# Kernel optimization log

Measured on AMD Instinct MI355X. Metric: run time of the kernel, lower is better.

Reference implementation:

```python
import jax, jax.numpy as jnp
import numpy as np

H = 50      # hidden_size (fixed in source)
IN = 7      # input_size = len(features)
B = 1024    # batch
T = 512     # seq_len
FC1 = 25
OUT = 1


def setup_inputs() -> dict:
    key = jax.random.key(0)
    ks = jax.random.split(key, 24)
    s = 1.0 / np.sqrt(H)  # PyTorch LSTM/Linear default uniform init scale

    def u(k, shape):
        return jax.random.uniform(k, shape, jnp.float32, -s, s)

    d = {"x": jax.random.normal(ks[0], (B, T, IN), jnp.float32)}
    # 4 stacked LSTM layers total: lstm1 has 2 layers (in=7 then 50), lstm2 has 2 layers (in=50)
    in_sizes = [IN, H, H, H]
    for l, isz in enumerate(in_sizes):
        d[f"Wih{l}"] = u(ks[1 + 4 * l], (4 * H, isz))
        d[f"Whh{l}"] = u(ks[2 + 4 * l], (4 * H, H))
        d[f"bih{l}"] = u(ks[3 + 4 * l], (4 * H,))
        d[f"bhh{l}"] = u(ks[4 + 4 * l], (4 * H,))
    d["W1"] = u(ks[17], (FC1, H))
    d["b1"] = u(ks[18], (FC1,))
    d["W2"] = u(ks[19], (OUT, FC1))
    d["b2"] = u(ks[20], (OUT,))
    return d


def _lstm_layer(x, Wih, Whh, bih, bhh):
    # x: [B, T, in] -> hidden sequence [B, T, H]. PyTorch gate order: i, f, g, o.
    b, t, _ = x.shape
    h = Whh.shape[1]
    # Precompute input projection for all timesteps in one big GEMM: [T, B, 4H]
    xp = jnp.einsum('bti,gi->tbg', x, Wih) + (bih + bhh)

    def step(carry, xt):
        hs, cs = carry
        gates = xt + hs @ Whh.T                      # [B, 4H]
        i, f, g, o = jnp.split(gates, 4, axis=-1)
        i = jax.nn.sigmoid(i)
        f = jax.nn.sigmoid(f)
        g = jnp.tanh(g)
        o = jax.nn.sigmoid(o)
        cs = f * cs + i * g
        hs = o * jnp.tanh(cs)
        return (hs, cs), hs

    h0 = jnp.zeros((b, h), x.dtype)
    _, hseq = jax.lax.scan(step, (h0, h0), xp)       # hseq: [T, B, H]
    return hseq.transpose(1, 0, 2)


def reference(x, Wih0, Whh0, bih0, bhh0, Wih1, Whh1, bih1, bhh1,
              Wih2, Whh2, bih2, bhh2, Wih3, Whh3, bih3, bhh3,
              W1, b1, W2, b2):
    out = x
    layers = [(Wih0, Whh0, bih0, bhh0), (Wih1, Whh1, bih1, bhh1),
              (Wih2, Whh2, bih2, bhh2), (Wih3, Whh3, bih3, bhh3)]
    for Wih, Whh, bih, bhh in layers:
        out = _lstm_layer(out, Wih, Whh, bih, bhh)
    h = out[:, -1, :]                                # last timestep [B, H]
    # dropout is identity in eval mode
    h = jax.nn.relu(h @ W1.T + b1)
    return h @ W2.T + b2                             # [B, 1]
```

## Files before the change

### kernel.cpp

```cpp
#include <hip/hip_runtime.h>


#define H 50
#define INSZ 7
#define TT 512
#define NL 4
#define FC1N 25
#define BPG 4
#define NBLK 256
#define NTHREADS 1024
#define HS 80
#define BIASL 56

typedef _Float16 half_t;
typedef __attribute__((ext_vector_type(8))) _Float16 half8_t;
typedef __attribute__((ext_vector_type(4))) float float4_t;

struct Params {
  const float* x;
  const float* Wih[NL];
  const float* Whh[NL];
  const float* bih[NL];
  const float* bhh[NL];
  const float* W1;
  const float* b1;
  const float* W2;
  const float* b2;
  float* out;
};

#define MFMA16(A, B, C) __builtin_amdgcn_mfma_f32_16x16x32_f16((A), (B), (C), 0, 0, 0)
#define EXP2F(x) __builtin_amdgcn_exp2f(x)
#define RCPF(x) __builtin_amdgcn_rcpf(x)

__global__ __launch_bounds__(NTHREADS, 4) void lstm_r10(Params p) {
  __shared__ __align__(16) half_t Xpack[2][BPG][HS];
  __shared__ __align__(16) half_t Hbuf[3][2][BPG][HS];
  __shared__ __align__(16) half_t Xstage[64][BPG][8];
  __shared__ float fc_h[BPG][H];
  __shared__ float fc1_buf[BPG][FC1N];

  const int tid = threadIdx.x;
  const int b0 = blockIdx.x * BPG;
  const int lane = tid & 63;
  const int quad = lane >> 4;
  const int col = lane & 15;
  const int glay = tid >> 8;
  const int wl = (((tid >> 6) & 3) + glay) & 3;

  half8_t afrag[4][4];
#pragma unroll
  for (int t4 = 0; t4 < 4; ++t4) {
#pragma unroll
    for (int g = 0; g < 4; ++g) {
      half8_t v;
#pragma unroll
      for (int j = 0; j < 8; ++j) {
        const int r = wl * 64 + t4 * 16 + col;
        const int u = r >> 2, q = r & 3;
        const int k = g * 32 + quad * 8 + j;
        float wv = 0.0f;
        if (u < H) {
          const int row = q * H + u;
          if (glay == 0) {
            if (k < INSZ) wv = p.Wih[0][row * INSZ + k];
            else if (k == 7) wv = p.bih[0][row] + p.bhh[0][row];
            else if (k >= 8 && k < 8 + H) wv = p.Whh[0][row * H + (k - 8)];
          } else if (glay == 1) {
            if (k == 7) wv = p.bih[1][row] + p.bhh[1][row];
            else if (k >= 8 && k < 8 + H) wv = p.Wih[1][row * H + (k - 8)];
            else if (k >= 64 && k < 64 + H) wv = p.Whh[1][row * H + (k - 64)];
          } else {
            if (k < H) wv = p.Wih[glay][row * H + k];
            else if (k == BIASL) wv = p.bih[glay][row] + p.bhh[glay][row];
            else if (k >= 64 && k < 64 + H) wv = p.Whh[glay][row * H + (k - 64)];
          }
          wv *= (q == 2) ? -2.885390082f : -1.442695041f;
        }
        v[j] = (half_t)wv;
      }
      afrag[t4][g] = v;
    }
  }

  {
    unsigned* xz = (unsigned*)Xpack;
    for (int i = tid; i < 2 * BPG * HS / 2; i += NTHREADS) xz[i] = 0u;
    unsigned* hz = (unsigned*)Hbuf;
    for (int i = tid; i < 3 * 2 * BPG * HS / 2; i += NTHREADS) hz[i] = 0u;
  }
  __syncthreads();
  if (tid < 8) {
    Xpack[tid >> 2][tid & 3][7] = (half_t)1.0f;
  } else if (tid < 8 + 24) {
    const int i = tid - 8, l = i >> 3, pr = (i >> 2) & 1, b = i & 3;
    Hbuf[l][pr][b][BIASL] = (half_t)1.0f;
  }
  for (int i = tid; i < 64 * BPG * INSZ; i += NTHREADS) {
    const int t = i / (BPG * INSZ), rem = i % (BPG * INSZ);
    const int b = rem / INSZ, k = rem % INSZ;
    const half_t xh = (half_t)p.x[((size_t)(b0 + b) * TT + t) * INSZ + k];
    Xstage[t][b][k] = xh;
    if (t == 0) Xpack[0][b][k] = xh;
  }
  __syncthreads();

  const int bb = col & 3;
  const int tsel = col >> 2;
  const int uu = 16 * wl + 4 * tsel + quad;
  const bool updact = (uu < H);

  const half_t* pin2[2];
  const half_t* pown2[2];
  half_t* pst2[2];
  if (glay == 0) {
    pin2[0] = &Xpack[0][bb][quad * 8];
    pin2[1] = &Xpack[1][bb][quad * 8];
    pown2[0] = pin2[0];
    pown2[1] = pin2[1];
    pst2[0] = &Xpack[1][bb][8 + uu];
    pst2[1] = &Xpack[0][bb][8 + uu];
  } else if (glay == 1) {
    pin2[0] = &Xpack[0][bb][quad * 8];
    pin2[1] = &Xpack[1][bb][quad * 8];
    pown2[0] = &Hbuf[0][0][bb][quad * 8];
    pown2[1] = &Hbuf[0][1][bb][quad * 8];
    pst2[0] = &Hbuf[0][1][bb][uu];
    pst2[1] = &Hbuf[0][0][bb][uu];
  } else {
    pin2[0] = &Hbuf[glay - 2][0][bb][quad * 8];
    pin2[1] = &Hbuf[glay - 2][1][bb][quad * 8];
    pown2[0] = &Hbuf[glay - 1][0][bb][quad * 8];
    pown2[1] = &Hbuf[glay - 1][1][bb][quad * 8];
    pst2[0] = &Hbuf[glay - 1][1][bb][uu];
    pst2[1] = &Hbuf[glay - 1][0][bb][uu];
  }
  const half_t* in_e = pin2[0];
  const half_t* in_o = pin2[1];
  const half_t* own_e = pown2[0];
  const half_t* own_o = pown2[1];
  half_t* st_e = pst2[0];
  half_t* st_o = pst2[1];

  const bool xwave = (glay == 0) && (wl == 3);
  const bool xcopy = xwave && (lane < BPG * INSZ);
  const int cb = lane / INSZ, ck = lane % INSZ;
  const int rb = lane >> 5;
  const int rt = lane & 31;

  float cst = 0.0f;
  const float4_t fzc = {0.0f, 0.0f, 0.0f, 0.0f};

#define TICK_BODY(PIN, POWN, PST, FCW)                                          \
  {                                                                             \
    float4_t a0, a1, a2, a3;                                                    \
    if (glay == 0) {                                                            \
      const half8_t v0 = *(const half8_t*)(PIN);                                \
      const half8_t v1 = *(const half8_t*)((PIN) + 32);                         \
      __builtin_amdgcn_s_setprio(1);                                            \
      if (wl != 3) {                                                            \
        a0 = MFMA16(afrag[0][0], v0, fzc); a1 = MFMA16(afrag[1][0], v0, fzc);   \
        a2 = MFMA16(afrag[2][0], v0, fzc); a3 = MFMA16(afrag[3][0], v0, fzc);   \
        a0 = MFMA16(afrag[0][1], v1, a0); a1 = MFMA16(afrag[1][1], v1, a1);     \
        a2 = MFMA16(afrag[2][1], v1, a2); a3 = MFMA16(afrag[3][1], v1, a3);     \
      } else {                                                                  \
        a0 = MFMA16(afrag[0][0], v0, fzc);                                      \
        a0 = MFMA16(afrag[0][1], v1, a0);                                       \
        a1 = a0; a2 = a0; a3 = a0;                                              \
      }                                                                         \
      __builtin_amdgcn_s_setprio(0);                                            \
    } else {                                                                    \
      const half8_t v0 = *(const half8_t*)(PIN);                                \
      const half8_t v1 = *(const half8_t*)((PIN) + 32);                         \
      const half8_t v2 = *(const half8_t*)(POWN);                               \
      const half8_t v3 = *(const half8_t*)((POWN) + 32);                        \
      __builtin_amdgcn_s_setprio(1);                                            \
      if (wl != 3) {                                                            \
        a0 = MFMA16(afrag[0][0], v0, fzc); a1 = MFMA16(afrag[1][0], v0, fzc);   \
        a2 = MFMA16(afrag[2][0], v0, fzc); a3 = MFMA16(afrag[3][0], v0, fzc);   \
        a0 = MFMA16(afrag[0][1], v1, a0); a1 = MFMA16(afrag[1][1], v1, a1);     \
        a2 = MFMA16(afrag[2][1], v1, a2); a3 = MFMA16(afrag[3][1], v1, a3);     \
        a0 = MFMA16(afrag[0][2], v2, a0); a1 = MFMA16(afrag[1][2], v2, a1);     \
        a2 = MFMA16(afrag[2][2], v2, a2); a3 = MFMA16(afrag[3][2], v2, a3);     \
        a0 = MFMA16(afrag[0][3], v3, a0); a1 = MFMA16(afrag[1][3], v3, a1);     \
        a2 = MFMA16(afrag[2][3], v3, a2); a3 = MFMA16(afrag[3][3], v3, a3);     \
      } else {                                                                  \
        a0 = MFMA16(afrag[0][0], v0, fzc);                                      \
        a0 = MFMA16(afrag[0][1], v1, a0);                                       \
        a0 = MFMA16(afrag[0][2], v2, a0);                                       \
        a0 = MFMA16(afrag[0][3], v3, a0);                                       \
        a1 = a0; a2 = a0; a3 = a0;                                              \
      }                                                                         \
      __builtin_amdgcn_s_setprio(0);                                            \
    }                                                                           \
    if (updact) {                                                               \
      const float4_t g01 = (col & 4) ? a1 : a0;                                 \
      const float4_t g23 = (col & 4) ? a3 : a2;                                 \
      const float4_t ga = (col & 8) ? g23 : g01;                                \
      const float di = 1.0f + EXP2F(ga[0]);                                     \
      const float df = 1.0f + EXP2F(ga[1]);                                     \
      const float dg = 1.0f + EXP2F(ga[2]);                                     \
      const float dq = 1.0f + EXP2F(ga[3]);                                     \
      const float r1 = RCPF(di * df);                                           \
      const float r2 = RCPF(dg * dq);                                           \
      const float gi = r1 * df;                                                 \
      const float gf = r1 * di;                                                 \
      const float gg = 2.0f * (r2 * dq) - 1.0f;                                 \
      const float go = r2 * dg;                                                 \
      cst = gf * cst + gi * gg;                                                 \
      const float dc = 1.0f + EXP2F(-2.885390082f * cst);                       \
      const float h = go * (2.0f * RCPF(dc) - 1.0f);                            \
      *(PST) = (half_t)h;                                                       \
      if (FCW) fc_h[bb][uu] = h;                                                \
    }                                                                           \
  }

#define XCOPY(S)                                                                \
  if (xcopy) {                                                                  \
    const int tn = (S) + 1;                                                     \
    Xpack[tn & 1][cb][ck] = Xstage[tn & 63][cb][ck];                            \
  }

  for (int s = 0; s < 3; ++s) {
    const int t = s - glay;
    if (t >= 0) {
      const int ph = s & 1;
      TICK_BODY(pin2[ph], pown2[ph], pst2[ph], false)
    }
    XCOPY(s)
    __syncthreads();
  }

  for (int s = 3; s < 511; s += 2) {
    {
      TICK_BODY(in_o, own_o, st_o, false)
      XCOPY(s)
    }
    __syncthreads();
    {
      const int s2 = s + 1;
      if (xwave && (s2 & 31) == 8 && s2 < 480) {
        const int tb = (s2 & ~31) + 32;
#pragma unroll
        for (int pp = 0; pp < 2; ++pp) {
          const int b = rb + 2 * pp;
          const int t = tb + rt;
          const float* src = &p.x[((size_t)(b0 + b) * TT + t) * INSZ];
          half_t* dst = &Xstage[t & 63][b][0];
#pragma unroll
          for (int k = 0; k < INSZ; ++k) dst[k] = (half_t)src[k];
        }
      }
      TICK_BODY(in_e, own_e, st_e, false)
      XCOPY(s2)
    }
    __syncthreads();
  }

  for (int s = 511; s < TT + NL - 1; ++s) {
    const int t = s - glay;
    if (t < TT) {
      const int ph = s & 1;
      const bool fcw = (glay == NL - 1) && (t == TT - 1);
      TICK_BODY(pin2[ph], pown2[ph], pst2[ph], fcw)
    }
    __syncthreads();
  }

  if (tid < BPG * FC1N) {
    const int b = tid / FC1N, j = tid % FC1N;
    const float* w = p.W1 + j * H;
    float a = p.b1[j];
#pragma unroll
    for (int k = 0; k < H; ++k) a += fc_h[b][k] * w[k];
    fc1_buf[b][j] = fmaxf(a, 0.0f);
  }
  __syncthreads();
  if (tid < BPG) {
    float a = p.b2[0];
#pragma unroll
    for (int j = 0; j < FC1N; ++j) a += fc1_buf[tid][j] * p.W2[j];
    p.out[b0 + tid] = a;
  }
}

extern "C" void kernel_launch(void* const* d_in, const int* in_sizes, int n_in,
                              void* d_out, int out_size, void* d_ws, size_t ws_size,
                              hipStream_t stream) {
  Params p;
  p.x = (const float*)d_in[0];
  for (int l = 0; l < NL; ++l) {
    p.Wih[l] = (const float*)d_in[1 + 4 * l];
    p.Whh[l] = (const float*)d_in[2 + 4 * l];
    p.bih[l] = (const float*)d_in[3 + 4 * l];
    p.bhh[l] = (const float*)d_in[4 + 4 * l];
  }
  p.W1 = (const float*)d_in[17];
  p.b1 = (const float*)d_in[18];
  p.W2 = (const float*)d_in[19];
  p.b2 = (const float*)d_in[20];
  p.out = (float*)d_out;

  hipLaunchKernelGGL(lstm_r10, dim3(NBLK), dim3(NTHREADS), 0, stream, p);
}
```

Measured before the change: 478.0 us.

## Replace per-tick block barriers with per-layer LDS counters and triple buffering

Drops the __syncthreads after every wavefront tick. Each layer group now spins on shared-memory progress counters that its neighbouring layers bump with atomics, and the hidden and input buffers go from double to triple buffering so layers can drift by one step. The goal is to let the four layer groups run loosely coupled instead of lock-stepping the whole 1024-thread block. The x staging ring shrinks to 32 entries with a 16-step refill, and the final hidden state is read straight from the ring buffer in fp16. The risks are spin-wait overhead, fragile memory ordering, and a small precision change in the FC input.

```diff
diff --git a/kernel.cpp b/kernel.cpp
--- a/kernel.cpp
+++ b/kernel.cpp
@@ -33,11 +33,11 @@
 #define EXP2F(x) __builtin_amdgcn_exp2f(x)
 #define RCPF(x) __builtin_amdgcn_rcpf(x)
 
-__global__ __launch_bounds__(NTHREADS, 4) void lstm_r10(Params p) {
-  __shared__ __align__(16) half_t Xpack[2][BPG][HS];
-  __shared__ __align__(16) half_t Hbuf[3][2][BPG][HS];
-  __shared__ __align__(16) half_t Xstage[64][BPG][8];
-  __shared__ float fc_h[BPG][H];
+__global__ __launch_bounds__(NTHREADS, 4) void lstm_r13(Params p) {
+  __shared__ __align__(16) half_t XP[3][BPG][HS];
+  __shared__ __align__(16) half_t Hb[3][3][BPG][HS];
+  __shared__ __align__(16) half_t Xstage[32][BPG][8];
+  __shared__ int prodc[16];
   __shared__ float fc1_buf[BPG][FC1N];
 
   const int tid = threadIdx.x;
@@ -84,24 +84,25 @@
   }
 
   {
-    unsigned* xz = (unsigned*)Xpack;
-    for (int i = tid; i < 2 * BPG * HS / 2; i += NTHREADS) xz[i] = 0u;
-    unsigned* hz = (unsigned*)Hbuf;
-    for (int i = tid; i < 3 * 2 * BPG * HS / 2; i += NTHREADS) hz[i] = 0u;
-  }
-  __syncthreads();
-  if (tid < 8) {
-    Xpack[tid >> 2][tid & 3][7] = (half_t)1.0f;
-  } else if (tid < 8 + 24) {
-    const int i = tid - 8, l = i >> 3, pr = (i >> 2) & 1, b = i & 3;
-    Hbuf[l][pr][b][BIASL] = (half_t)1.0f;
-  }
-  for (int i = tid; i < 64 * BPG * INSZ; i += NTHREADS) {
+    unsigned* xz = (unsigned*)XP;
+    for (int i = tid; i < 3 * BPG * HS / 2; i += NTHREADS) xz[i] = 0u;
+    unsigned* hz = (unsigned*)Hb;
+    for (int i = tid; i < 3 * 3 * BPG * HS / 2; i += NTHREADS) hz[i] = 0u;
+    if (tid < 16) prodc[tid] = 0;
+  }
+  __syncthreads();
+  if (tid < 12) {
+    XP[tid >> 2][tid & 3][7] = (half_t)1.0f;
+  } else if (tid < 12 + 36) {
+    const int i = tid - 12, l = i / 12, pr = (i >> 2) % 3, b = i & 3;
+    Hb[l][pr][b][BIASL] = (half_t)1.0f;
+  }
+  for (int i = tid; i < 32 * BPG * INSZ; i += NTHREADS) {
     const int t = i / (BPG * INSZ), rem = i % (BPG * INSZ);
     const int b = rem / INSZ, k = rem % INSZ;
     const half_t xh = (half_t)p.x[((size_t)(b0 + b) * TT + t) * INSZ + k];
     Xstage[t][b][k] = xh;
-    if (t == 0) Xpack[0][b][k] = xh;
+    if (t == 0) XP[2][b][k] = xh;
   }
   __syncthreads();
 
@@ -110,48 +111,70 @@
   const int uu = 16 * wl + 4 * tsel + quad;
   const bool updact = (uu < H);
 
-  const half_t* pin2[2];
-  const half_t* pown2[2];
-  half_t* pst2[2];
-  if (glay == 0) {
-    pin2[0] = &Xpack[0][bb][quad * 8];
-    pin2[1] = &Xpack[1][bb][quad * 8];
-    pown2[0] = pin2[0];
-    pown2[1] = pin2[1];
-    pst2[0] = &Xpack[1][bb][8 + uu];
-    pst2[1] = &Xpack[0][bb][8 + uu];
-  } else if (glay == 1) {
-    pin2[0] = &Xpack[0][bb][quad * 8];
-    pin2[1] = &Xpack[1][bb][quad * 8];
-    pown2[0] = &Hbuf[0][0][bb][quad * 8];
-    pown2[1] = &Hbuf[0][1][bb][quad * 8];
-    pst2[0] = &Hbuf[0][1][bb][uu];
-    pst2[1] = &Hbuf[0][0][bb][uu];
-  } else {
-    pin2[0] = &Hbuf[glay - 2][0][bb][quad * 8];
-    pin2[1] = &Hbuf[glay - 2][1][bb][quad * 8];
-    pown2[0] = &Hbuf[glay - 1][0][bb][quad * 8];
-    pown2[1] = &Hbuf[glay - 1][1][bb][quad * 8];
-    pst2[0] = &Hbuf[glay - 1][1][bb][uu];
-    pst2[1] = &Hbuf[glay - 1][0][bb][uu];
-  }
-  const half_t* in_e = pin2[0];
-  const half_t* in_o = pin2[1];
-  const half_t* own_e = pown2[0];
-  const half_t* own_o = pown2[1];
-  half_t* st_e = pst2[0];
-  half_t* st_o = pst2[1];
+  const half_t* pin3[3];
+  const half_t* pown3[3];
+  half_t* pst3[3];
+#pragma unroll
+  for (int pp = 0; pp < 3; ++pp) {
+    if (glay == 0) {
+      pin3[pp] = &XP[pp][bb][quad * 8];
+      pown3[pp] = pin3[pp];
+      pst3[pp] = &XP[pp][bb][8 + uu];
+    } else if (glay == 1) {
+      pin3[pp] = &XP[pp][bb][quad * 8];
+      pown3[pp] = &Hb[0][pp][bb][quad * 8];
+      pst3[pp] = &Hb[0][pp][bb][uu];
+    } else {
+      pin3[pp] = &Hb[glay - 2][pp][bb][quad * 8];
+      pown3[pp] = &Hb[glay - 1][pp][bb][quad * 8];
+      pst3[pp] = &Hb[glay - 1][pp][bb][uu];
+    }
+  }
+  const half_t* pinT[3] = {glay ? pin3[0] : pin3[2],
+                           glay ? pin3[1] : pin3[0],
+                           glay ? pin3[2] : pin3[1]};
+  const half_t* pownT[3] = {pown3[2], pown3[0], pown3[1]};
 
   const bool xwave = (glay == 0) && (wl == 3);
   const bool xcopy = xwave && (lane < BPG * INSZ);
   const int cb = lane / INSZ, ck = lane % INSZ;
-  const int rb = lane >> 5;
-  const int rt = lane & 31;
 
   float cst = 0.0f;
   const float4_t fzc = {0.0f, 0.0f, 0.0f, 0.0f};
-
-#define TICK_BODY(PIN, POWN, PST, FCW)                                          \
+  volatile int* pv = (volatile int*)prodc;
+
+#define WAITT(T_)                                                               \
+  {                                                                             \
+    const int bS = 4 * (T_);                                                    \
+    if (glay == 0) {                                                            \
+      while (pv[0] < bS || pv[1] < bS - 4) {}                                   \
+    } else if (glay == 1) {                                                     \
+      while (pv[1] < bS || pv[0] < bS + 4 || pv[2] < bS - 4) {}                 \
+    } else if (glay == 2) {                                                     \
+      while (pv[2] < bS || pv[1] < bS + 4 || pv[3] < bS - 4) {}                 \
+    } else {                                                                    \
+      while (pv[3] < bS || pv[2] < bS + 4) {}                                   \
+    }                                                                           \
+    __builtin_amdgcn_sched_barrier(0);                                          \
+    asm volatile("" ::: "memory");                                              \
+  }
+
+#define DONE()                                                                  \
+  {                                                                             \
+    asm volatile("s_waitcnt lgkmcnt(0)" ::: "memory");                          \
+    if (lane == 0) atomicAdd(&prodc[glay], 1);                                  \
+  }
+
+#define REFILL(T_)                                                              \
+  if (xwave && ((T_)&15) == 0 && (T_) > 0 && (T_) + 16 < TT) {                  \
+    const int t0 = (T_) + 16 + (lane >> 2);                                     \
+    const int rb = lane & 3;                                                    \
+    const float* src = &p.x[((size_t)(b0 + rb) * TT + t0) * INSZ];              \
+    half_t* dst = &Xstage[t0 & 31][rb][0];                                      \
+    _Pragma("unroll") for (int k = 0; k < INSZ; ++k) dst[k] = (half_t)src[k];   \
+  }
+
+#define TICK3(PIN, POWN, PST)                                                   \
   {                                                                             \
     float4_t a0, a1, a2, a3;                                                    \
     if (glay == 0) {                                                            \
@@ -211,68 +234,34 @@
       const float dc = 1.0f + EXP2F(-2.885390082f * cst);                       \
       const float h = go * (2.0f * RCPF(dc) - 1.0f);                            \
       *(PST) = (half_t)h;                                                       \
-      if (FCW) fc_h[bb][uu] = h;                                                \
     }                                                                           \
   }
 
-#define XCOPY(S)                                                                \
-  if (xcopy) {                                                                  \
-    const int tn = (S) + 1;                                                     \
-    Xpack[tn & 1][cb][ck] = Xstage[tn & 63][cb][ck];                            \
-  }
-
-  for (int s = 0; s < 3; ++s) {
-    const int t = s - glay;
-    if (t >= 0) {
-      const int ph = s & 1;
-      TICK_BODY(pin2[ph], pown2[ph], pst2[ph], false)
-    }
-    XCOPY(s)
-    __syncthreads();
-  }
-
-  for (int s = 3; s < 511; s += 2) {
-    {
-      TICK_BODY(in_o, own_o, st_o, false)
-      XCOPY(s)
-    }
-    __syncthreads();
-    {
-      const int s2 = s + 1;
-      if (xwave && (s2 & 31) == 8 && s2 < 480) {
-        const int tb = (s2 & ~31) + 32;
-#pragma unroll
-        for (int pp = 0; pp < 2; ++pp) {
-          const int b = rb + 2 * pp;
-          const int t = tb + rt;
-          const float* src = &p.x[((size_t)(b0 + b) * TT + t) * INSZ];
-          half_t* dst = &Xstage[t & 63][b][0];
-#pragma unroll
-          for (int k = 0; k < INSZ; ++k) dst[k] = (half_t)src[k];
-        }
-      }
-      TICK_BODY(in_e, own_e, st_e, false)
-      XCOPY(s2)
-    }
-    __syncthreads();
-  }
-
-  for (int s = 511; s < TT + NL - 1; ++s) {
-    const int t = s - glay;
-    if (t < TT) {
-      const int ph = s & 1;
-      const bool fcw = (glay == NL - 1) && (t == TT - 1);
-      TICK_BODY(pin2[ph], pown2[ph], pst2[ph], fcw)
-    }
-    __syncthreads();
-  }
+#define STEP(T_, P_)                                                            \
+  {                                                                             \
+    WAITT(T_)                                                                   \
+    TICK3(pinT[P_], pownT[P_], pst3[P_])                                        \
+    if (xcopy && (T_) + 1 < TT)                                                 \
+      XP[P_][cb][ck] = Xstage[((T_) + 1) & 31][cb][ck];                         \
+    DONE()                                                                      \
+    REFILL(T_)                                                                  \
+  }
+
+  for (int T = 0; T < 510; T += 3) {
+    STEP(T, 0)
+    STEP(T + 1, 1)
+    STEP(T + 2, 2)
+  }
+  STEP(510, 0)
+  STEP(511, 1)
+  __syncthreads();
 
   if (tid < BPG * FC1N) {
     const int b = tid / FC1N, j = tid % FC1N;
     const float* w = p.W1 + j * H;
     float a = p.b1[j];
 #pragma unroll
-    for (int k = 0; k < H; ++k) a += fc_h[b][k] * w[k];
+    for (int k = 0; k < H; ++k) a += (float)Hb[2][1][b][k] * w[k];
     fc1_buf[b][j] = fmaxf(a, 0.0f);
   }
   __syncthreads();
@@ -301,5 +290,5 @@
   p.b2 = (const float*)d_in[20];
   p.out = (float*)d_out;
 
-  hipLaunchKernelGGL(lstm_r10, dim3(NBLK), dim3(NTHREADS), 0, stream, p);
+  hipLaunchKernelGGL(lstm_r13, dim3(NBLK), dim3(NTHREADS), 0, stream, p);
 }
```

Result: slower. 559.9 us (+17.1%).

## Repartition LSTM gates across 2 waves per layer instead of 4

Applied to the files above, without the earlier changes.

Halves the block to 512 threads, giving each layer two waves. Each wave now owns 7 MFMA column tiles and updates two hidden units per lane, with two cell states. The old layout used four waves per layer, one of them mostly idle, so the change should cut wasted waves and barrier participants per tick. In exchange each wave issues more serial MFMAs per tick, holds 28 fragment registers, and does twice the activation math, which lengthens the per-step critical path.

```diff
diff --git a/kernel.cpp b/kernel.cpp
--- a/kernel.cpp
+++ b/kernel.cpp
@@ -8,7 +8,7 @@
 #define FC1N 25
 #define BPG 4
 #define NBLK 256
-#define NTHREADS 1024
+#define NTHREADS 512
 #define HS 80
 #define BIASL 56
 
@@ -33,8 +33,23 @@
 #define EXP2F(x) __builtin_amdgcn_exp2f(x)
 #define RCPF(x) __builtin_amdgcn_rcpf(x)
 
-__global__ __launch_bounds__(NTHREADS, 4) void lstm_r10(Params p) {
-  __shared__ __align__(16) half_t Xpack[2][BPG][HS];
+#define UPD(g, c, h)                                                     \
+  const float di = 1.0f + EXP2F((g)[0]);                                 \
+  const float df = 1.0f + EXP2F((g)[1]);                                 \
+  const float dgg = 1.0f + EXP2F((g)[2]);                                \
+  const float dq = 1.0f + EXP2F((g)[3]);                                 \
+  const float r1 = RCPF(di * df);                                        \
+  const float r2 = RCPF(dgg * dq);                                       \
+  const float gi = r1 * df;                                              \
+  const float gf = r1 * di;                                              \
+  const float gg = 2.0f * (r2 * dq) - 1.0f;                              \
+  const float go = r2 * dgg;                                             \
+  (c) = gf * (c) + gi * gg;                                              \
+  const float dc = 1.0f + EXP2F(-2.885390082f * (c));                    \
+  const float h = go * (2.0f * RCPF(dc) - 1.0f);
+
+__global__ __launch_bounds__(NTHREADS, 2) void lstm_r14(Params p) {
+  __shared__ __align__(16) half_t XP[2][BPG][HS];
   __shared__ __align__(16) half_t Hbuf[3][2][BPG][HS];
   __shared__ __align__(16) half_t Xstage[64][BPG][8];
   __shared__ float fc_h[BPG][H];
@@ -45,53 +60,59 @@
   const int lane = tid & 63;
   const int quad = lane >> 4;
   const int col = lane & 15;
-  const int glay = tid >> 8;
-  const int wl = (((tid >> 6) & 3) + glay) & 3;
-
-  half8_t afrag[4][4];
-#pragma unroll
-  for (int t4 = 0; t4 < 4; ++t4) {
-#pragma unroll
-    for (int g = 0; g < 4; ++g) {
-      half8_t v;
-#pragma unroll
-      for (int j = 0; j < 8; ++j) {
-        const int r = wl * 64 + t4 * 16 + col;
-        const int u = r >> 2, q = r & 3;
-        const int k = g * 32 + quad * 8 + j;
-        float wv = 0.0f;
-        if (u < H) {
-          const int row = q * H + u;
-          if (glay == 0) {
-            if (k < INSZ) wv = p.Wih[0][row * INSZ + k];
-            else if (k == 7) wv = p.bih[0][row] + p.bhh[0][row];
-            else if (k >= 8 && k < 8 + H) wv = p.Whh[0][row * H + (k - 8)];
-          } else if (glay == 1) {
-            if (k == 7) wv = p.bih[1][row] + p.bhh[1][row];
-            else if (k >= 8 && k < 8 + H) wv = p.Wih[1][row * H + (k - 8)];
-            else if (k >= 64 && k < 64 + H) wv = p.Whh[1][row * H + (k - 64)];
-          } else {
-            if (k < H) wv = p.Wih[glay][row * H + k];
-            else if (k == BIASL) wv = p.bih[glay][row] + p.bhh[glay][row];
-            else if (k >= 64 && k < 64 + H) wv = p.Whh[glay][row * H + (k - 64)];
+  const int w = tid >> 6;
+  const int glay = w >> 1;
+  const int hf = w & 1;
+  const int cb0 = hf * 7;
+  const int bb = col & 3;
+  const int tsel = col >> 2;
+
+  half8_t af[7][4];
+  {
+    const int q = col & 3;
+#pragma unroll
+    for (int lcc = 0; lcc < 7; ++lcc) {
+      const int u = (cb0 + lcc) * 4 + tsel;
+#pragma unroll
+      for (int kg = 0; kg < 4; ++kg) {
+        half8_t v;
+#pragma unroll
+        for (int j = 0; j < 8; ++j) {
+          const int k = kg * 32 + quad * 8 + j;
+          float wv = 0.0f;
+          if (u < H) {
+            const int row = q * H + u;
+            if (glay == 0) {
+              if (k < INSZ) wv = p.Wih[0][row * INSZ + k];
+              else if (k == 7) wv = p.bih[0][row] + p.bhh[0][row];
+              else if (k >= 8 && k < 8 + H) wv = p.Whh[0][row * H + (k - 8)];
+            } else if (glay == 1) {
+              if (k == 7) wv = p.bih[1][row] + p.bhh[1][row];
+              else if (k >= 8 && k < 8 + H) wv = p.Wih[1][row * H + (k - 8)];
+              else if (k >= 64 && k < 64 + H) wv = p.Whh[1][row * H + (k - 64)];
+            } else {
+              if (k < H) wv = p.Wih[glay][row * H + k];
+              else if (k == BIASL) wv = p.bih[glay][row] + p.bhh[glay][row];
+              else if (k >= 64 && k < 64 + H) wv = p.Whh[glay][row * H + (k - 64)];
+            }
+            wv *= (q == 2) ? -2.885390082f : -1.442695041f;
           }
-          wv *= (q == 2) ? -2.885390082f : -1.442695041f;
+          v[j] = (half_t)wv;
         }
-        v[j] = (half_t)wv;
+        af[lcc][kg] = v;
       }
-      afrag[t4][g] = v;
     }
   }
 
   {
-    unsigned* xz = (unsigned*)Xpack;
+    unsigned* xz = (unsigned*)XP;
     for (int i = tid; i < 2 * BPG * HS / 2; i += NTHREADS) xz[i] = 0u;
     unsigned* hz = (unsigned*)Hbuf;
     for (int i = tid; i < 3 * 2 * BPG * HS / 2; i += NTHREADS) hz[i] = 0u;
   }
   __syncthreads();
   if (tid < 8) {
-    Xpack[tid >> 2][tid & 3][7] = (half_t)1.0f;
+    XP[tid >> 2][tid & 3][7] = (half_t)1.0f;
   } else if (tid < 8 + 24) {
     const int i = tid - 8, l = i >> 3, pr = (i >> 2) & 1, b = i & 3;
     Hbuf[l][pr][b][BIASL] = (half_t)1.0f;
@@ -101,39 +122,38 @@
     const int b = rem / INSZ, k = rem % INSZ;
     const half_t xh = (half_t)p.x[((size_t)(b0 + b) * TT + t) * INSZ + k];
     Xstage[t][b][k] = xh;
-    if (t == 0) Xpack[0][b][k] = xh;
+    if (t == 0) XP[0][b][k] = xh;
   }
   __syncthreads();
 
-  const int bb = col & 3;
-  const int tsel = col >> 2;
-  const int uu = 16 * wl + 4 * tsel + quad;
-  const bool updact = (uu < H);
+  const int u0c = (cb0 + tsel) * 4 + quad;
+  const int u1c = u0c + 16;
+  const bool r1ok = ((4 + tsel) < (7 - hf)) && (u1c < H);
 
   const half_t* pin2[2];
   const half_t* pown2[2];
   half_t* pst2[2];
   if (glay == 0) {
-    pin2[0] = &Xpack[0][bb][quad * 8];
-    pin2[1] = &Xpack[1][bb][quad * 8];
+    pin2[0] = &XP[0][bb][quad * 8];
+    pin2[1] = &XP[1][bb][quad * 8];
     pown2[0] = pin2[0];
     pown2[1] = pin2[1];
-    pst2[0] = &Xpack[1][bb][8 + uu];
-    pst2[1] = &Xpack[0][bb][8 + uu];
+    pst2[0] = &XP[1][bb][8];
+    pst2[1] = &XP[0][bb][8];
   } else if (glay == 1) {
-    pin2[0] = &Xpack[0][bb][quad * 8];
-    pin2[1] = &Xpack[1][bb][quad * 8];
+    pin2[0] = &XP[0][bb][quad * 8];
+    pin2[1] = &XP[1][bb][quad * 8];
     pown2[0] = &Hbuf[0][0][bb][quad * 8];
     pown2[1] = &Hbuf[0][1][bb][quad * 8];
-    pst2[0] = &Hbuf[0][1][bb][uu];
-    pst2[1] = &Hbuf[0][0][bb][uu];
+    pst2[0] = &Hbuf[0][1][bb][0];
+    pst2[1] = &Hbuf[0][0][bb][0];
   } else {
     pin2[0] = &Hbuf[glay - 2][0][bb][quad * 8];
     pin2[1] = &Hbuf[glay - 2][1][bb][quad * 8];
     pown2[0] = &Hbuf[glay - 1][0][bb][quad * 8];
     pown2[1] = &Hbuf[glay - 1][1][bb][quad * 8];
-    pst2[0] = &Hbuf[glay - 1][1][bb][uu];
-    pst2[1] = &Hbuf[glay - 1][0][bb][uu];
+    pst2[0] = &Hbuf[glay - 1][1][bb][0];
+    pst2[1] = &Hbuf[glay - 1][0][bb][0];
   }
   const half_t* in_e = pin2[0];
   const half_t* in_o = pin2[1];
@@ -142,83 +162,86 @@
   half_t* st_e = pst2[0];
   half_t* st_o = pst2[1];
 
-  const bool xwave = (glay == 0) && (wl == 3);
+  const bool xwave = (w == 1);
   const bool xcopy = xwave && (lane < BPG * INSZ);
   const int cb = lane / INSZ, ck = lane % INSZ;
   const int rb = lane >> 5;
   const int rt = lane & 31;
 
-  float cst = 0.0f;
+  float cst0 = 0.0f, cst1 = 0.0f;
   const float4_t fzc = {0.0f, 0.0f, 0.0f, 0.0f};
 
-#define TICK_BODY(PIN, POWN, PST, FCW)                                          \
+#define TICK_BODY(PIN, POWN, STB, FCW)                                          \
   {                                                                             \
-    float4_t a0, a1, a2, a3;                                                    \
+    const half8_t v0 = *(const half8_t*)(PIN);                                  \
+    const half8_t v1 = *(const half8_t*)((PIN) + 32);                           \
+    float4_t a0, a1, a2, a3, a4, a5, a6;                                        \
     if (glay == 0) {                                                            \
-      const half8_t v0 = *(const half8_t*)(PIN);                                \
-      const half8_t v1 = *(const half8_t*)((PIN) + 32);                         \
       __builtin_amdgcn_s_setprio(1);                                            \
-      if (wl != 3) {                                                            \
-        a0 = MFMA16(afrag[0][0], v0, fzc); a1 = MFMA16(afrag[1][0], v0, fzc);   \
-        a2 = MFMA16(afrag[2][0], v0, fzc); a3 = MFMA16(afrag[3][0], v0, fzc);   \
-        a0 = MFMA16(afrag[0][1], v1, a0); a1 = MFMA16(afrag[1][1], v1, a1);     \
-        a2 = MFMA16(afrag[2][1], v1, a2); a3 = MFMA16(afrag[3][1], v1, a3);     \
+      a0 = MFMA16(af[0][0], v0, fzc); a1 = MFMA16(af[1][0], v0, fzc);           \
+      a2 = MFMA16(af[2][0], v0, fzc); a3 = MFMA16(af[3][0], v0, fzc);           \
+      a4 = MFMA16(af[4][0], v0, fzc); a5 = MFMA16(af[5][0], v0, fzc);           \
+      a0 = MFMA16(af[0][1], v1, a0);  a1 = MFMA16(af[1][1], v1, a1);            \
+      a2 = MFMA16(af[2][1], v1, a2);  a3 = MFMA16(af[3][1], v1, a3);            \
+      a4 = MFMA16(af[4][1], v1, a4);  a5 = MFMA16(af[5][1], v1, a5);            \
+      if (hf == 0) {                                                            \
+        a6 = MFMA16(af[6][0], v0, fzc);                                         \
+        a6 = MFMA16(af[6][1], v1, a6);                                          \
       } else {                                                                  \
-        a0 = MFMA16(afrag[0][0], v0, fzc);                                      \
-        a0 = MFMA16(afrag[0][1], v1, a0);                                       \
-        a1 = a0; a2 = a0; a3 = a0;                                              \
+        a6 = a5;                                                                \
       }                                                                         \
       __builtin_amdgcn_s_setprio(0);                                            \
     } else {                                                                    \
-      const half8_t v0 = *(const half8_t*)(PIN);                                \
-      const half8_t v1 = *(const half8_t*)((PIN) + 32);                         \
       const half8_t v2 = *(const half8_t*)(POWN);                               \
       const half8_t v3 = *(const half8_t*)((POWN) + 32);                        \
       __builtin_amdgcn_s_setprio(1);                                            \
-      if (wl != 3) {                                                            \
-        a0 = MFMA16(afrag[0][0], v0, fzc); a1 = MFMA16(afrag[1][0], v0, fzc);   \
-        a2 = MFMA16(afrag[2][0], v0, fzc); a3 = MFMA16(afrag[3][0], v0, fzc);   \
-        a0 = MFMA16(afrag[0][1], v1, a0); a1 = MFMA16(afrag[1][1], v1, a1);     \
-        a2 = MFMA16(afrag[2][1], v1, a2); a3 = MFMA16(afrag[3][1], v1, a3);     \
-        a0 = MFMA16(afrag[0][2], v2, a0); a1 = MFMA16(afrag[1][2], v2, a1);     \
-        a2 = MFMA16(afrag[2][2], v2, a2); a3 = MFMA16(afrag[3][2], v2, a3);     \
-        a0 = MFMA16(afrag[0][3], v3, a0); a1 = MFMA16(afrag[1][3], v3, a1);     \
-        a2 = MFMA16(afrag[2][3], v3, a2); a3 = MFMA16(afrag[3][3], v3, a3);     \
+      a0 = MFMA16(af[0][0], v0, fzc); a1 = MFMA16(af[1][0], v0, fzc);           \
+      a2 = MFMA16(af[2][0], v0, fzc); a3 = MFMA16(af[3][0], v0, fzc);           \
+      a4 = MFMA16(af[4][0], v0, fzc); a5 = MFMA16(af[5][0], v0, fzc);           \
+      a0 = MFMA16(af[0][1], v1, a0);  a1 = MFMA16(af[1][1], v1, a1);            \
+      a2 = MFMA16(af[2][1], v1, a2);  a3 = MFMA16(af[3][1], v1, a3);            \
+      a4 = MFMA16(af[4][1], v1, a4);  a5 = MFMA16(af[5][1], v1, a5);            \
+      a0 = MFMA16(af[0][2], v2, a0);  a1 = MFMA16(af[1][2], v2, a1);            \
+      a2 = MFMA16(af[2][2], v2, a2);  a3 = MFMA16(af[3][2], v2, a3);            \
+      a4 = MFMA16(af[4][2], v2, a4);  a5 = MFMA16(af[5][2], v2, a5);            \
+      a0 = MFMA16(af[0][3], v3, a0);  a1 = MFMA16(af[1][3], v3, a1);            \
+      a2 = MFMA16(af[2][3], v3, a2);  a3 = MFMA16(af[3][3], v3, a3);            \
+      a4 = MFMA16(af[4][3], v3, a4);  a5 = MFMA16(af[5][3], v3, a5);            \
+      if (hf == 0) {                                                            \
+        a6 = MFMA16(af[6][0], v0, fzc);                                         \
+        a6 = MFMA16(af[6][1], v1, a6);                                          \
+        a6 = MFMA16(af[6][2], v2, a6);                                          \
+        a6 = MFMA16(af[6][3], v3, a6);                                          \
       } else {                                                                  \
-        a0 = MFMA16(afrag[0][0], v0, fzc);                                      \
-        a0 = MFMA16(afrag[0][1], v1, a0);                                       \
-        a0 = MFMA16(afrag[0][2], v2, a0);                                       \
-        a0 = MFMA16(afrag[0][3], v3, a0);                                       \
-        a1 = a0; a2 = a0; a3 = a0;                                              \
+        a6 = a5;                                                                \
       }                                                                         \
       __builtin_amdgcn_s_setprio(0);                                            \
     }                                                                           \
-    if (updact) {                                                               \
-      const float4_t g01 = (col & 4) ? a1 : a0;                                 \
-      const float4_t g23 = (col & 4) ? a3 : a2;                                 \
-      const float4_t ga = (col & 8) ? g23 : g01;                                \
-      const float di = 1.0f + EXP2F(ga[0]);                                     \
-      const float df = 1.0f + EXP2F(ga[1]);                                     \
-      const float dg = 1.0f + EXP2F(ga[2]);                                     \
-      const float dq = 1.0f + EXP2F(ga[3]);                                     \
-      const float r1 = RCPF(di * df);                                           \
-      const float r2 = RCPF(dg * dq);                                           \
-      const float gi = r1 * df;                                                 \
-      const float gf = r1 * di;                                                 \
-      const float gg = 2.0f * (r2 * dq) - 1.0f;                                 \
-      const float go = r2 * dg;                                                 \
-      cst = gf * cst + gi * gg;                                                 \
-      const float dc = 1.0f + EXP2F(-2.885390082f * cst);                       \
-      const float h = go * (2.0f * RCPF(dc) - 1.0f);                            \
-      *(PST) = (half_t)h;                                                       \
-      if (FCW) fc_h[bb][uu] = h;                                                \
+                                      \
+    const float4_t x01 = (tsel & 1) ? a1 : a0;                                  \
+    const float4_t x23 = (tsel & 1) ? a3 : a2;                                  \
+    const float4_t o0 = (tsel & 2) ? x23 : x01;                                 \
+    {                                                                           \
+      UPD(o0, cst0, h0v)                                                        \
+      (STB)[u0c] = (half_t)h0v;                                                 \
+      if (FCW) fc_h[bb][u0c] = h0v;                                             \
+    }                                                                           \
+                     \
+    const float4_t y45 = (tsel & 1) ? a5 : a4;                                  \
+    const float4_t o1 = (tsel & 2) ? a6 : y45;                                  \
+    {                                                                           \
+      UPD(o1, cst1, h1v)                                                        \
+      if (r1ok) {                                                               \
+        (STB)[u1c] = (half_t)h1v;                                               \
+        if (FCW) fc_h[bb][u1c] = h1v;                                           \
+      }                                                                         \
     }                                                                           \
   }
 
 #define XCOPY(S)                                                                \
   if (xcopy) {                                                                  \
     const int tn = (S) + 1;                                                     \
-    Xpack[tn & 1][cb][ck] = Xstage[tn & 63][cb][ck];                            \
+    XP[tn & 1][cb][ck] = Xstage[tn & 63][cb][ck];                               \
   }
 
   for (int s = 0; s < 3; ++s) {
@@ -269,10 +292,10 @@
 
   if (tid < BPG * FC1N) {
     const int b = tid / FC1N, j = tid % FC1N;
-    const float* w = p.W1 + j * H;
+    const float* wgt = p.W1 + j * H;
     float a = p.b1[j];
 #pragma unroll
-    for (int k = 0; k < H; ++k) a += fc_h[b][k] * w[k];
+    for (int k = 0; k < H; ++k) a += fc_h[b][k] * wgt[k];
     fc1_buf[b][j] = fmaxf(a, 0.0f);
   }
   __syncthreads();
@@ -301,5 +324,5 @@
   p.b2 = (const float*)d_in[20];
   p.out = (float*)d_out;
 
-  hipLaunchKernelGGL(lstm_r10, dim3(NBLK), dim3(NTHREADS), 0, stream, p);
+  hipLaunchKernelGGL(lstm_r14, dim3(NBLK), dim3(NTHREADS), 0, stream, p);
 }
```

After: 509.9 us. 6.7% more time.
